# Kernel tuning notes

Hardware: AMD Instinct MI355X
Metric: run time of the kernel (lower is better)

Reference implementation:

```python
import jax, jax.numpy as jnp
import numpy as np

N = 50000   # nodes
E = 800000  # edges (before self loops)
IN_DIM = 64
HID = 128
HEADS = 4
DH = HID // HEADS  # 32 per-head out_feats
L = 3
EPS = 1e-5
NEG_SLOPE = 0.2


def setup_inputs() -> dict:
    key = jax.random.key(0)
    ks = jax.random.split(key, 10)
    s = 0.1  # weight scale for numerical sanity
    return {
        "node_feats": jax.random.normal(ks[0], (N, IN_DIM), jnp.float32),
        "src": jax.random.randint(ks[1], (E,), 0, N, dtype=jnp.int32),
        "dst": jax.random.randint(ks[2], (E,), 0, N, dtype=jnp.int32),
        "W_in": jax.random.normal(ks[3], (IN_DIM, HID), jnp.float32) * s,
        "b_in": jnp.zeros((HID,), jnp.float32),
        "W_src": jax.random.normal(ks[4], (L, HID, HID), jnp.float32) * s,
        "b_src": jnp.zeros((L, HID), jnp.float32),
        "W_dst": jax.random.normal(ks[5], (L, HID, HID), jnp.float32) * s,
        "b_dst": jnp.zeros((L, HID), jnp.float32),
        "attn": jax.random.normal(ks[6], (L, HEADS, DH), jnp.float32) * s,
        "ln_g": jnp.ones((L, HID), jnp.float32),
        "ln_b": jnp.zeros((L, HID), jnp.float32),
    }


def _layer_norm(x, g, b):
    mu = jnp.mean(x, axis=-1, keepdims=True)
    var = jnp.mean((x - mu) ** 2, axis=-1, keepdims=True)
    return (x - mu) * jax.lax.rsqrt(var + EPS) * g + b


def _gatv2(h, s_idx, d_idx, Ws, bs, Wd, bd, a):
    # h: [N, HID]; edges s_idx -> d_idx (self loops included)
    fs = (h @ Ws + bs).reshape(N, HEADS, DH)  # W_src h, source features
    fd = (h @ Wd + bd).reshape(N, HEADS, DH)  # W_dst h, dest features
    e = jax.nn.leaky_relu(fs[s_idx] + fd[d_idx], NEG_SLOPE)   # [E', H, D]
    logits = jnp.einsum('ehd,hd->eh', e, a)                   # [E', H]
    # segment softmax over incoming edges of each destination node
    m = jax.ops.segment_max(logits, d_idx, num_segments=N)    # [N, H]
    p = jnp.exp(logits - m[d_idx])
    z = jax.ops.segment_sum(p, d_idx, num_segments=N)         # [N, H]
    alpha = p / z[d_idx]                                      # [E', H]
    msg = fs[s_idx] * alpha[..., None]                        # [E', H, D]
    out = jax.ops.segment_sum(msg, d_idx, num_segments=N)     # [N, H, D]
    out = out + h.reshape(N, HEADS, DH)  # residual (Identity res_fc)
    return out.reshape(N, HID)


def reference(node_feats, src, dst, W_in, b_in, W_src, b_src, W_dst, b_dst, attn, ln_g, ln_b):
    loop = jnp.arange(N, dtype=src.dtype)
    s_idx = jnp.concatenate([src, loop])  # add_self_loop
    d_idx = jnp.concatenate([dst, loop])
    h = node_feats @ W_in + b_in
    for l in range(L):
        h_new = _gatv2(h, s_idx, d_idx, W_src[l], b_src[l], W_dst[l], b_dst[l], attn[l])
        h = _layer_norm(h + h_new, ln_g[l], ln_b[l])
        h = jax.nn.relu(h)
    graph_emb = jnp.mean(h, axis=0, keepdims=True)  # dgl.mean_nodes, batch of 1 graph
    return graph_emb, h
```

## Files before the change

kernel.cpp:

```cpp
#include <hip/hip_runtime.h>
#include <hip/hip_bf16.h>

#define NN 50000
#define CSTRIDE 16

typedef short short8 __attribute__((ext_vector_type(8)));
typedef float f32x4 __attribute__((ext_vector_type(4)));

#define GLOBAL_AS __attribute__((address_space(1)))
#define LDS_AS __attribute__((address_space(3)))

__device__ __forceinline__ unsigned short f2bf(float f) {
    unsigned int b = __float_as_uint(f);
    unsigned int r = (b + 0x7FFFu + ((b >> 16) & 1u)) >> 16;
    return (unsigned short)r;
}
__device__ __forceinline__ float bf2f(unsigned short u) {
    return __uint_as_float((unsigned int)u << 16);
}


__global__ __launch_bounds__(256, 4) void prep_kernel(
        const int* __restrict__ dst, int* countsS, int* __restrict__ rank, int E,
        const float* __restrict__ Ws, const float* __restrict__ Wd,
        unsigned short* __restrict__ WtL,
        const float* __restrict__ x, const float* __restrict__ Win,
        const float* __restrict__ bin, unsigned short* __restrict__ hB) {
    int HB = (E + 255) >> 8;
    int blk = blockIdx.x;
    if (blk < HB) {
        int i = blk * 256 + threadIdx.x;
        if (i < E) rank[i] = atomicAdd(&countsS[(size_t)dst[i] * CSTRIDE], 1);
        return;
    }
    if (blk < HB + 384) {
        int e = (blk - HB) * 256 + threadIdx.x;
        int l = e >> 15;
        int r = e & 32767;
        int colc = r >> 7;
        int k = r & 127;
        float v = (colc < 128) ? Ws[l * 16384 + k * 128 + colc]
                               : Wd[l * 16384 + k * 128 + (colc - 128)];
        WtL[l * 32768 + colc * 128 + k] = f2bf(v);
        return;
    }
    int blk0 = blk - HB - 384;
    int tid = threadIdx.x;
    int w = tid >> 6, l = tid & 63;
    int m = l & 15, q = l >> 4;
    short8 B[2][2];
    #pragma unroll
    for (int ct = 0; ct < 2; ++ct) {
        int colw = w * 32 + ct * 16 + m;
        #pragma unroll
        for (int kt = 0; kt < 2; ++kt) {
            short8 a;
            #pragma unroll
            for (int jj = 0; jj < 8; ++jj)
                a[jj] = (short)f2bf(Win[(kt * 32 + q * 8 + jj) * 128 + colw]);
            B[ct][kt] = a;
        }
    }
    float bias[2];
    #pragma unroll
    for (int ct = 0; ct < 2; ++ct) bias[ct] = bin[w * 32 + ct * 16 + m];
    for (int rg = blk0; rg < NN / 16; rg += 512) {
        int row0 = rg * 16;
        const float* ap = x + (size_t)(row0 + m) * 64 + q * 8;
        short8 A[2];
        #pragma unroll
        for (int kt = 0; kt < 2; ++kt) {
            float4 f0 = *(const float4*)(ap + kt * 32);
            float4 f1 = *(const float4*)(ap + kt * 32 + 4);
            short8 a;
            a[0] = (short)f2bf(f0.x); a[1] = (short)f2bf(f0.y);
            a[2] = (short)f2bf(f0.z); a[3] = (short)f2bf(f0.w);
            a[4] = (short)f2bf(f1.x); a[5] = (short)f2bf(f1.y);
            a[6] = (short)f2bf(f1.z); a[7] = (short)f2bf(f1.w);
            A[kt] = a;
        }
        f32x4 acc[2];
        #pragma unroll
        for (int ct = 0; ct < 2; ++ct) acc[ct] = (f32x4){0.f, 0.f, 0.f, 0.f};
        #pragma unroll
        for (int kt = 0; kt < 2; ++kt)
            #pragma unroll
            for (int ct = 0; ct < 2; ++ct)
                acc[ct] = __builtin_amdgcn_mfma_f32_16x16x32_bf16(A[kt], B[ct][kt], acc[ct], 0, 0, 0);
        #pragma unroll
        for (int ct = 0; ct < 2; ++ct) {
            int colw = w * 32 + ct * 16 + m;
            #pragma unroll
            for (int i = 0; i < 4; ++i) {
                int row = row0 + q * 4 + i;
                hB[(size_t)row * 128 + colw] = f2bf(acc[ct][i] + bias[ct]);
            }
        }
    }
}

__global__ __launch_bounds__(256) void alloc_kernel(const int* __restrict__ countsS,
                                                    int* __restrict__ row_beg,
                                                    int* total, int n) {
    int i = blockIdx.x * blockDim.x + threadIdx.x;
    int lane = threadIdx.x & 63;
    int len = (i < n) ? (countsS[(size_t)i * CSTRIDE] + 1) : 0;
    int p = len;
    #pragma unroll
    for (int off = 1; off < 64; off <<= 1) {
        int t = __shfl_up(p, off);
        if (lane >= off) p += t;
    }
    int tot = __shfl(p, 63);
    int base = 0;
    if (lane == 63) base = atomicAdd(total, tot);
    base = __shfl(base, 63);
    if (i < n) row_beg[i] = base + p - len;
}

__device__ __forceinline__ void dual_body(const unsigned short* __restrict__ hB,
                                          const unsigned short* __restrict__ Wt,
                                          const float* __restrict__ bs,
                                          const float* __restrict__ bd,
                                          unsigned short* __restrict__ fsB,
                                          unsigned short* __restrict__ fdB,
                                          unsigned short* Atile, int t0, int tstride) {
    int tid = threadIdx.x;
    int w = tid >> 6, l = tid & 63;
    int m = l & 15, q = l >> 4;
    short8 B[4][4];
    #pragma unroll
    for (int ct = 0; ct < 4; ++ct) {
        int colw = w * 64 + ct * 16 + m;
        const unsigned short* wp = Wt + colw * 128 + q * 8;
        #pragma unroll
        for (int kt = 0; kt < 4; ++kt) B[ct][kt] = *(const short8*)(wp + kt * 32);
    }
    const float* bptr = (w < 2) ? bs : bd;
    unsigned short* OUT = (w < 2) ? fsB : fdB;
    int ocb = (w * 64) & 127;
    float bias[4];
    #pragma unroll
    for (int ct = 0; ct < 4; ++ct) bias[ct] = bptr[ocb + ct * 16 + m];

    const int NT = (NN + 63) / 64;
    for (int t = t0; t < NT; t += tstride) {
        int row0 = t * 64;
        const char* gsrc = (const char*)(hB + (size_t)row0 * 128);
        #pragma unroll
        for (int c = 0; c < 4; ++c) {
            int off = c * 4096 + tid * 16;
            __builtin_amdgcn_global_load_lds((const GLOBAL_AS void*)(gsrc + off),
                                             (LDS_AS void*)((char*)Atile + off), 16, 0, 0);
        }
        __syncthreads();
        #pragma unroll
        for (int rg = 0; rg < 4; ++rg) {
            const unsigned short* ap = Atile + (rg * 16 + m) * 128 + q * 8;
            short8 A[4];
            #pragma unroll
            for (int kt = 0; kt < 4; ++kt) A[kt] = *(const short8*)(ap + kt * 32);
            f32x4 acc[4];
            #pragma unroll
            for (int ct = 0; ct < 4; ++ct) acc[ct] = (f32x4){0.f, 0.f, 0.f, 0.f};
            #pragma unroll
            for (int kt = 0; kt < 4; ++kt)
                #pragma unroll
                for (int ct = 0; ct < 4; ++ct)
                    acc[ct] = __builtin_amdgcn_mfma_f32_16x16x32_bf16(A[kt], B[ct][kt], acc[ct], 0, 0, 0);
            #pragma unroll
            for (int ct = 0; ct < 4; ++ct) {
                int colw = ocb + ct * 16 + m;
                #pragma unroll
                for (int i = 0; i < 4; ++i) {
                    int row = row0 + rg * 16 + q * 4 + i;
                    if (row < NN) OUT[(size_t)row * 128 + colw] = f2bf(acc[ct][i] + bias[ct]);
                }
            }
        }
        __syncthreads();
    }
}

__global__ __launch_bounds__(256, 4) void scatter_dual_kernel(
        const int* __restrict__ src, const int* __restrict__ dst,
        const int* __restrict__ rank, const int* __restrict__ row_beg,
        const int* __restrict__ countsS, int* __restrict__ col, int E, int n,
        const unsigned short* __restrict__ hB, const unsigned short* __restrict__ Wt,
        const float* __restrict__ bs, const float* __restrict__ bd,
        unsigned short* __restrict__ fsB, unsigned short* __restrict__ fdB) {
    __shared__ unsigned short Atile[64 * 128];
    int SB = (E + n + 255) >> 8;
    if ((int)blockIdx.x < SB) {
        int i = blockIdx.x * 256 + threadIdx.x;
        if (i >= E + n) return;
        if (i < E) {
            col[row_beg[dst[i]] + rank[i]] = src[i];
        } else {
            int v = i - E;
            col[row_beg[v] + countsS[(size_t)v * CSTRIDE]] = v;
        }
        return;
    }
    dual_body(hB, Wt, bs, bd, fsB, fdB, Atile, blockIdx.x - SB, gridDim.x - SB);
}

__global__ __launch_bounds__(256, 4) void dual_gemm_mfma(const unsigned short* __restrict__ hB,
                                                         const unsigned short* __restrict__ Wt,
                                                         const float* __restrict__ bs,
                                                         const float* __restrict__ bd,
                                                         unsigned short* __restrict__ fsB,
                                                         unsigned short* __restrict__ fdB) {
    __shared__ unsigned short Atile[64 * 128];
    dual_body(hB, Wt, bs, bd, fsB, fdB, Atile, blockIdx.x, gridDim.x);
}

__global__ __launch_bounds__(256) void agg_ln_kernel(const unsigned short* __restrict__ h_in,
                                                     const unsigned short* __restrict__ fsB,
                                                     const unsigned short* __restrict__ fdB,
                                                     const int* __restrict__ row_beg,
                                                     const int* __restrict__ countsS,
                                                     const int* __restrict__ col,
                                                     const float* __restrict__ attn,
                                                     const float* __restrict__ ln_g,
                                                     const float* __restrict__ ln_b,
                                                     unsigned short* __restrict__ hb_out,
                                                     float* __restrict__ hf_out, int n) {
    int gwave = (blockIdx.x * blockDim.x + threadIdx.x) >> 6;
    int lane = threadIdx.x & 63;
    int half = lane >> 5;
    int sub = lane & 31;
    int node = gwave * 2 + half;
    if (node >= n) return;
    int f0 = 4 * sub;
    unsigned foff = (unsigned)(f0 * 2);
    const char* fsp = (const char*)fsB;
    ushort4 ud = *(const ushort4*)((const char*)fdB + (((unsigned)node << 8) | foff));
    float4 fd4;
    fd4.x = bf2f(ud.x); fd4.y = bf2f(ud.y); fd4.z = bf2f(ud.z); fd4.w = bf2f(ud.w);
    ushort4 uh = *(const ushort4*)((const char*)h_in + (((unsigned)node << 8) | foff));
    float4 h4;
    h4.x = bf2f(uh.x); h4.y = bf2f(uh.y); h4.z = bf2f(uh.z); h4.w = bf2f(uh.w);
    const float4 a4 = *(const float4*)(attn + f0);
    float4 a06, a04;
    a06.x = 0.6f * a4.x; a06.y = 0.6f * a4.y; a06.z = 0.6f * a4.z; a06.w = 0.6f * a4.w;
    a04.x = 0.4f * a4.x; a04.y = 0.4f * a4.y; a04.z = 0.4f * a4.z; a04.w = 0.4f * a4.w;
    int beg = row_beg[node], end = beg + countsS[(size_t)node * CSTRIDE] + 1;

    float z[4];
    float4 acc[4];
    #pragma unroll
    for (int k = 0; k < 4; ++k) {
        z[k] = 0.f;
        acc[k].x = 0.f; acc[k].y = 0.f; acc[k].z = 0.f; acc[k].w = 0.f;
    }

    int j = beg;
    for (; j + 3 < end; j += 4) {
        int s0 = col[j], s1 = col[j + 1], s2 = col[j + 2], s3 = col[j + 3];
        ushort4 u0 = *(const ushort4*)(fsp + (((unsigned)s0 << 8) | foff));
        ushort4 u1 = *(const ushort4*)(fsp + (((unsigned)s1 << 8) | foff));
        ushort4 u2 = *(const ushort4*)(fsp + (((unsigned)s2 << 8) | foff));
        ushort4 u3 = *(const ushort4*)(fsp + (((unsigned)s3 << 8) | foff));
        float4 v0, v1, v2, v3;
        v0.x = bf2f(u0.x); v0.y = bf2f(u0.y); v0.z = bf2f(u0.z); v0.w = bf2f(u0.w);
        v1.x = bf2f(u1.x); v1.y = bf2f(u1.y); v1.z = bf2f(u1.z); v1.w = bf2f(u1.w);
        v2.x = bf2f(u2.x); v2.y = bf2f(u2.y); v2.z = bf2f(u2.z); v2.w = bf2f(u2.w);
        v3.x = bf2f(u3.x); v3.y = bf2f(u3.y); v3.z = bf2f(u3.z); v3.w = bf2f(u3.w);
        float p0, p1, p2, p3;
        {
            float e0 = v0.x + fd4.x, e1 = v0.y + fd4.y, e2 = v0.z + fd4.z, e3 = v0.w + fd4.w;
            p0 = e0 * a06.x + fabsf(e0) * a04.x + e1 * a06.y + fabsf(e1) * a04.y
               + e2 * a06.z + fabsf(e2) * a04.z + e3 * a06.w + fabsf(e3) * a04.w;
        }
        {
            float e0 = v1.x + fd4.x, e1 = v1.y + fd4.y, e2 = v1.z + fd4.z, e3 = v1.w + fd4.w;
            p1 = e0 * a06.x + fabsf(e0) * a04.x + e1 * a06.y + fabsf(e1) * a04.y
               + e2 * a06.z + fabsf(e2) * a04.z + e3 * a06.w + fabsf(e3) * a04.w;
        }
        {
            float e0 = v2.x + fd4.x, e1 = v2.y + fd4.y, e2 = v2.z + fd4.z, e3 = v2.w + fd4.w;
            p2 = e0 * a06.x + fabsf(e0) * a04.x + e1 * a06.y + fabsf(e1) * a04.y
               + e2 * a06.z + fabsf(e2) * a04.z + e3 * a06.w + fabsf(e3) * a04.w;
        }
        {
            float e0 = v3.x + fd4.x, e1 = v3.y + fd4.y, e2 = v3.z + fd4.z, e3 = v3.w + fd4.w;
            p3 = e0 * a06.x + fabsf(e0) * a04.x + e1 * a06.y + fabsf(e1) * a04.y
               + e2 * a06.z + fabsf(e2) * a04.z + e3 * a06.w + fabsf(e3) * a04.w;
        }
        #pragma unroll
        for (int off = 1; off <= 4; off <<= 1) {
            p0 += __shfl_xor(p0, off);
            p1 += __shfl_xor(p1, off);
            p2 += __shfl_xor(p2, off);
            p3 += __shfl_xor(p3, off);
        }
        float w0 = __expf(p0), w1 = __expf(p1), w2 = __expf(p2), w3 = __expf(p3);
        z[0] += w0; z[1] += w1; z[2] += w2; z[3] += w3;
        acc[0].x += w0 * v0.x; acc[0].y += w0 * v0.y; acc[0].z += w0 * v0.z; acc[0].w += w0 * v0.w;
        acc[1].x += w1 * v1.x; acc[1].y += w1 * v1.y; acc[1].z += w1 * v1.z; acc[1].w += w1 * v1.w;
        acc[2].x += w2 * v2.x; acc[2].y += w2 * v2.y; acc[2].z += w2 * v2.z; acc[2].w += w2 * v2.w;
        acc[3].x += w3 * v3.x; acc[3].y += w3 * v3.y; acc[3].z += w3 * v3.z; acc[3].w += w3 * v3.w;
    }
    for (; j < end; ++j) {
        int s = col[j];
        ushort4 u = *(const ushort4*)(fsp + (((unsigned)s << 8) | foff));
        float4 v;
        v.x = bf2f(u.x); v.y = bf2f(u.y); v.z = bf2f(u.z); v.w = bf2f(u.w);
        float e0 = v.x + fd4.x, e1 = v.y + fd4.y, e2 = v.z + fd4.z, e3 = v.w + fd4.w;
        float p = e0 * a06.x + fabsf(e0) * a04.x + e1 * a06.y + fabsf(e1) * a04.y
                + e2 * a06.z + fabsf(e2) * a04.z + e3 * a06.w + fabsf(e3) * a04.w;
        p += __shfl_xor(p, 1);
        p += __shfl_xor(p, 2);
        p += __shfl_xor(p, 4);
        float w = __expf(p);
        z[0] += w;
        acc[0].x += w * v.x; acc[0].y += w * v.y; acc[0].z += w * v.z; acc[0].w += w * v.w;
    }
    float zT = (z[0] + z[1]) + (z[2] + z[3]);
    float axT = (acc[0].x + acc[1].x) + (acc[2].x + acc[3].x);
    float ayT = (acc[0].y + acc[1].y) + (acc[2].y + acc[3].y);
    float azT = (acc[0].z + acc[1].z) + (acc[2].z + acc[3].z);
    float awT = (acc[0].w + acc[1].w) + (acc[2].w + acc[3].w);
    float inv = 1.0f / zT;
    float x0 = 2.f * h4.x + axT * inv;
    float x1 = 2.f * h4.y + ayT * inv;
    float x2 = 2.f * h4.z + azT * inv;
    float x3 = 2.f * h4.w + awT * inv;
    float s = (x0 + x1) + (x2 + x3);
    #pragma unroll
    for (int off = 1; off <= 16; off <<= 1) s += __shfl_xor(s, off);
    float mean = s * (1.f / 128.f);
    float d0 = x0 - mean, d1 = x1 - mean, d2 = x2 - mean, d3 = x3 - mean;
    float v = (d0 * d0 + d1 * d1) + (d2 * d2 + d3 * d3);
    #pragma unroll
    for (int off = 1; off <= 16; off <<= 1) v += __shfl_xor(v, off);
    float rstd = rsqrtf(v * (1.f / 128.f) + 1e-5f);
    float4 g4 = *(const float4*)(ln_g + f0);
    float4 bb4 = *(const float4*)(ln_b + f0);
    float4 o;
    o.x = fmaxf(d0 * rstd * g4.x + bb4.x, 0.f);
    o.y = fmaxf(d1 * rstd * g4.y + bb4.y, 0.f);
    o.z = fmaxf(d2 * rstd * g4.z + bb4.z, 0.f);
    o.w = fmaxf(d3 * rstd * g4.w + bb4.w, 0.f);
    if (hf_out) {
        *(float4*)((char*)hf_out + (((unsigned)node << 9) | (unsigned)(f0 * 4))) = o;
    } else {
        ushort4 ob;
        ob.x = f2bf(o.x); ob.y = f2bf(o.y); ob.z = f2bf(o.z); ob.w = f2bf(o.w);
        *(ushort4*)((char*)hb_out + (((unsigned)node << 8) | foff)) = ob;
    }
}


__global__ __launch_bounds__(128) void mean1_kernel(const float* __restrict__ h,
                                                    float* __restrict__ partials, int n) {
    int c = threadIdx.x;
    float acc = 0.f;
    for (int r = blockIdx.x; r < n; r += gridDim.x)
        acc += h[(size_t)r * 128 + c];
    partials[blockIdx.x * 128 + c] = acc;
}

__global__ __launch_bounds__(1024) void mean2_kernel(const float* __restrict__ partials,
                                                     float* __restrict__ out, int nb, int n) {
    __shared__ float smem[8][128];
    int c = threadIdx.x & 127;
    int g = threadIdx.x >> 7;
    float acc = 0.f;
    for (int r = g; r < nb; r += 8)
        acc += partials[r * 128 + c];
    smem[g][c] = acc;
    __syncthreads();
    if (threadIdx.x < 128) {
        float s = 0.f;
        #pragma unroll
        for (int k = 0; k < 8; ++k) s += smem[k][c];
        out[c] = s * (1.f / n);
    }
}

extern "C" void kernel_launch(void* const* d_in, const int* in_sizes, int n_in,
                              void* d_out, int out_size, void* d_ws, size_t ws_size,
                              hipStream_t stream) {
    const float* node_feats = (const float*)d_in[0];
    const int* src = (const int*)d_in[1];
    const int* dst = (const int*)d_in[2];
    const float* W_in = (const float*)d_in[3];
    const float* b_in = (const float*)d_in[4];
    const float* W_src = (const float*)d_in[5];
    const float* b_src = (const float*)d_in[6];
    const float* W_dst = (const float*)d_in[7];
    const float* b_dst = (const float*)d_in[8];
    const float* attn = (const float*)d_in[9];
    const float* ln_g = (const float*)d_in[10];
    const float* ln_b = (const float*)d_in[11];
    float* out = (float*)d_out;

    const int N = NN;
    const int E = in_sizes[1];

    unsigned short* fsB = (unsigned short*)d_ws;
    unsigned short* fdB = fsB + (size_t)N * 128;
    unsigned short* hB = fdB + (size_t)N * 128;
    unsigned short* WtL = hB + (size_t)N * 128;
    unsigned short* WtIn = WtL + 3 * 32768;
    int* countsS = (int*)(WtIn + 8192);
    int* total = countsS + (size_t)N * CSTRIDE;
    int* row_beg = total + 1;
    int* rankb = row_beg + N;
    int* colb = rankb + E;
    float* partials = (float*)(colb + (E + N));

    const int NT = (N + 63) / 64;

    hipMemsetAsync(countsS, 0, ((size_t)N * CSTRIDE + 1) * sizeof(int), stream);
    int HB = (E + 255) / 256;
    prep_kernel<<<HB + 384 + 512, 256, 0, stream>>>(dst, countsS, rankb, E,
                                                    W_src, W_dst, WtL,
                                                    node_feats, W_in, b_in, hB);
    alloc_kernel<<<(N + 255) / 256, 256, 0, stream>>>(countsS, row_beg, total, N);

    int SB = (E + N + 255) / 256;
    scatter_dual_kernel<<<SB + NT, 256, 0, stream>>>(src, dst, rankb, row_beg,
                                                     countsS, colb, E, N,
                                                     hB, WtL, b_src, b_dst, fsB, fdB);

    for (int l = 0; l < 3; ++l) {
        int last = (l == 2);
        if (l > 0)
            dual_gemm_mfma<<<NT, 256, 0, stream>>>(hB, WtL + (size_t)l * 32768,
                                                   b_src + l * 128, b_dst + l * 128,
                                                   fsB, fdB);
        agg_ln_kernel<<<(N + 7) / 8, 256, 0, stream>>>(hB, fsB, fdB, row_beg, countsS, colb,
                                                       attn + l * 128, ln_g + l * 128,
                                                       ln_b + l * 128,
                                                       last ? nullptr : hB,
                                                       last ? (out + 128) : nullptr, N);
    }

    mean1_kernel<<<256, 128, 0, stream>>>(out + 128, partials, N);
    mean2_kernel<<<1, 1024, 0, stream>>>(partials, out, 256, N);
}
```

Measured before the change: 411.1 us.

## Fuse layer-0 projection into prep kernel, unroll edge loop by 8, merge mean kernels

The layer-0 dual GEMM moves into the first prep kernel. Those blocks recompute the input projection for their 64-row tile into shared memory and multiply it by W_src/W_dst read directly from fp32, so it no longer waits on the scatter kernel. The scatter becomes a standalone kernel. The aggregation loop gets an 8-edge unrolled stage to raise memory-level parallelism on the gathers. The two-stage mean reduction is replaced by one kernel that uses atomics on a zeroed output, which drops a launch but makes the summation order nondeterministic.

Measured after the change: 436.4 us. 6.1% more time.

```diff
diff --git a/kernel.cpp b/kernel.cpp
--- a/kernel.cpp
+++ b/kernel.cpp
@@ -18,82 +18,205 @@
 __device__ __forceinline__ float bf2f(unsigned short u) {
     return __uint_as_float((unsigned int)u << 16);
 }
-
-
-__global__ __launch_bounds__(256, 4) void prep_kernel(
+__device__ __forceinline__ float4 bfu4(ushort4 u) {
+    float4 v;
+    v.x = bf2f(u.x); v.y = bf2f(u.y); v.z = bf2f(u.z); v.w = bf2f(u.w);
+    return v;
+}
+__device__ __forceinline__ float edge_logit(float4 v, float4 fd4, float4 a06, float4 a04) {
+    float e0 = v.x + fd4.x, e1 = v.y + fd4.y, e2 = v.z + fd4.z, e3 = v.w + fd4.w;
+    return e0 * a06.x + fabsf(e0) * a04.x + e1 * a06.y + fabsf(e1) * a04.y
+         + e2 * a06.z + fabsf(e2) * a04.z + e3 * a06.w + fabsf(e3) * a04.w;
+}
+
+
+__global__ __launch_bounds__(256, 4) void mega0_kernel(
         const int* __restrict__ dst, int* countsS, int* __restrict__ rank, int E,
         const float* __restrict__ Ws, const float* __restrict__ Wd,
         unsigned short* __restrict__ WtL,
         const float* __restrict__ x, const float* __restrict__ Win,
-        const float* __restrict__ bin, unsigned short* __restrict__ hB) {
+        const float* __restrict__ bin, unsigned short* __restrict__ hB,
+        const float* __restrict__ bs0, const float* __restrict__ bd0,
+        unsigned short* __restrict__ fsB, unsigned short* __restrict__ fdB) {
+    __shared__ unsigned short Atile[64 * 128];
     int HB = (E + 255) >> 8;
     int blk = blockIdx.x;
+    int tid = threadIdx.x;
     if (blk < HB) {
-        int i = blk * 256 + threadIdx.x;
+        int i = blk * 256 + tid;
         if (i < E) rank[i] = atomicAdd(&countsS[(size_t)dst[i] * CSTRIDE], 1);
         return;
     }
-    if (blk < HB + 384) {
-        int e = (blk - HB) * 256 + threadIdx.x;
-        int l = e >> 15;
+    int w = tid >> 6, l = tid & 63;
+    int m = l & 15, q = l >> 4;
+    if (blk < HB + 512) {
+        int blk0 = blk - HB;
+        short8 B[2][2];
+        #pragma unroll
+        for (int ct = 0; ct < 2; ++ct) {
+            int colw = w * 32 + ct * 16 + m;
+            #pragma unroll
+            for (int kt = 0; kt < 2; ++kt) {
+                short8 a;
+                #pragma unroll
+                for (int jj = 0; jj < 8; ++jj)
+                    a[jj] = (short)f2bf(Win[(kt * 32 + q * 8 + jj) * 128 + colw]);
+                B[ct][kt] = a;
+            }
+        }
+        float bias[2];
+        #pragma unroll
+        for (int ct = 0; ct < 2; ++ct) bias[ct] = bin[w * 32 + ct * 16 + m];
+        for (int rg = blk0; rg < NN / 16; rg += 512) {
+            int row0 = rg * 16;
+            const float* ap = x + (size_t)(row0 + m) * 64 + q * 8;
+            short8 A[2];
+            #pragma unroll
+            for (int kt = 0; kt < 2; ++kt) {
+                float4 f0 = *(const float4*)(ap + kt * 32);
+                float4 f1 = *(const float4*)(ap + kt * 32 + 4);
+                short8 a;
+                a[0] = (short)f2bf(f0.x); a[1] = (short)f2bf(f0.y);
+                a[2] = (short)f2bf(f0.z); a[3] = (short)f2bf(f0.w);
+                a[4] = (short)f2bf(f1.x); a[5] = (short)f2bf(f1.y);
+                a[6] = (short)f2bf(f1.z); a[7] = (short)f2bf(f1.w);
+                A[kt] = a;
+            }
+            f32x4 acc[2];
+            #pragma unroll
+            for (int ct = 0; ct < 2; ++ct) acc[ct] = (f32x4){0.f, 0.f, 0.f, 0.f};
+            #pragma unroll
+            for (int kt = 0; kt < 2; ++kt)
+                #pragma unroll
+                for (int ct = 0; ct < 2; ++ct)
+                    acc[ct] = __builtin_amdgcn_mfma_f32_16x16x32_bf16(A[kt], B[ct][kt], acc[ct], 0, 0, 0);
+            #pragma unroll
+            for (int ct = 0; ct < 2; ++ct) {
+                int colw = w * 32 + ct * 16 + m;
+                #pragma unroll
+                for (int i = 0; i < 4; ++i) {
+                    int row = row0 + q * 4 + i;
+                    hB[(size_t)row * 128 + colw] = f2bf(acc[ct][i] + bias[ct]);
+                }
+            }
+        }
+        return;
+    }
+    if (blk < HB + 512 + 256) {
+        int e = (blk - HB - 512) * 256 + tid;
+        int ll = 1 + (e >> 15);
         int r = e & 32767;
         int colc = r >> 7;
         int k = r & 127;
-        float v = (colc < 128) ? Ws[l * 16384 + k * 128 + colc]
-                               : Wd[l * 16384 + k * 128 + (colc - 128)];
-        WtL[l * 32768 + colc * 128 + k] = f2bf(v);
+        float v = (colc < 128) ? Ws[ll * 16384 + k * 128 + colc]
+                               : Wd[ll * 16384 + k * 128 + (colc - 128)];
+        WtL[ll * 32768 + colc * 128 + k] = f2bf(v);
         return;
     }
-    int blk0 = blk - HB - 384;
-    int tid = threadIdx.x;
-    int w = tid >> 6, l = tid & 63;
-    int m = l & 15, q = l >> 4;
-    short8 B[2][2];
-    #pragma unroll
-    for (int ct = 0; ct < 2; ++ct) {
-        int colw = w * 32 + ct * 16 + m;
-        #pragma unroll
-        for (int kt = 0; kt < 2; ++kt) {
-            short8 a;
-            #pragma unroll
-            for (int jj = 0; jj < 8; ++jj)
-                a[jj] = (short)f2bf(Win[(kt * 32 + q * 8 + jj) * 128 + colw]);
-            B[ct][kt] = a;
-        }
-    }
-    float bias[2];
-    #pragma unroll
-    for (int ct = 0; ct < 2; ++ct) bias[ct] = bin[w * 32 + ct * 16 + m];
-    for (int rg = blk0; rg < NN / 16; rg += 512) {
-        int row0 = rg * 16;
-        const float* ap = x + (size_t)(row0 + m) * 64 + q * 8;
-        short8 A[2];
-        #pragma unroll
-        for (int kt = 0; kt < 2; ++kt) {
-            float4 f0 = *(const float4*)(ap + kt * 32);
-            float4 f1 = *(const float4*)(ap + kt * 32 + 4);
-            short8 a;
-            a[0] = (short)f2bf(f0.x); a[1] = (short)f2bf(f0.y);
-            a[2] = (short)f2bf(f0.z); a[3] = (short)f2bf(f0.w);
-            a[4] = (short)f2bf(f1.x); a[5] = (short)f2bf(f1.y);
-            a[6] = (short)f2bf(f1.z); a[7] = (short)f2bf(f1.w);
-            A[kt] = a;
-        }
-        f32x4 acc[2];
-        #pragma unroll
-        for (int ct = 0; ct < 2; ++ct) acc[ct] = (f32x4){0.f, 0.f, 0.f, 0.f};
-        #pragma unroll
-        for (int kt = 0; kt < 2; ++kt)
-            #pragma unroll
-            for (int ct = 0; ct < 2; ++ct)
-                acc[ct] = __builtin_amdgcn_mfma_f32_16x16x32_bf16(A[kt], B[ct][kt], acc[ct], 0, 0, 0);
+    int t = blk - (HB + 512 + 256);
+    int row0 = t * 64;
+    {
+        short8 BW[2][2];
         #pragma unroll
         for (int ct = 0; ct < 2; ++ct) {
             int colw = w * 32 + ct * 16 + m;
             #pragma unroll
-            for (int i = 0; i < 4; ++i) {
-                int row = row0 + q * 4 + i;
-                hB[(size_t)row * 128 + colw] = f2bf(acc[ct][i] + bias[ct]);
+            for (int kt = 0; kt < 2; ++kt) {
+                short8 a;
+                #pragma unroll
+                for (int jj = 0; jj < 8; ++jj)
+                    a[jj] = (short)f2bf(Win[(kt * 32 + q * 8 + jj) * 128 + colw]);
+                BW[ct][kt] = a;
+            }
+        }
+        float biasW[2];
+        #pragma unroll
+        for (int ct = 0; ct < 2; ++ct) biasW[ct] = bin[w * 32 + ct * 16 + m];
+        #pragma unroll
+        for (int rg = 0; rg < 4; ++rg) {
+            int row = row0 + rg * 16 + m;
+            short8 A1[2];
+            if (row < NN) {
+                const float* ap = x + (size_t)row * 64 + q * 8;
+                #pragma unroll
+                for (int kt = 0; kt < 2; ++kt) {
+                    float4 f0 = *(const float4*)(ap + kt * 32);
+                    float4 f1 = *(const float4*)(ap + kt * 32 + 4);
+                    short8 a;
+                    a[0] = (short)f2bf(f0.x); a[1] = (short)f2bf(f0.y);
+                    a[2] = (short)f2bf(f0.z); a[3] = (short)f2bf(f0.w);
+                    a[4] = (short)f2bf(f1.x); a[5] = (short)f2bf(f1.y);
+                    a[6] = (short)f2bf(f1.z); a[7] = (short)f2bf(f1.w);
+                    A1[kt] = a;
+                }
+            } else {
+                #pragma unroll
+                for (int kt = 0; kt < 2; ++kt) {
+                    short8 a;
+                    #pragma unroll
+                    for (int jj = 0; jj < 8; ++jj) a[jj] = 0;
+                    A1[kt] = a;
+                }
+            }
+            f32x4 acc2[2];
+            #pragma unroll
+            for (int ct = 0; ct < 2; ++ct) acc2[ct] = (f32x4){0.f, 0.f, 0.f, 0.f};
+            #pragma unroll
+            for (int kt = 0; kt < 2; ++kt)
+                #pragma unroll
+                for (int ct = 0; ct < 2; ++ct)
+                    acc2[ct] = __builtin_amdgcn_mfma_f32_16x16x32_bf16(A1[kt], BW[ct][kt], acc2[ct], 0, 0, 0);
+            #pragma unroll
+            for (int ct = 0; ct < 2; ++ct)
+                #pragma unroll
+                for (int i = 0; i < 4; ++i)
+                    Atile[(rg * 16 + q * 4 + i) * 128 + w * 32 + ct * 16 + m] =
+                        f2bf(acc2[ct][i] + biasW[ct]);
+        }
+    }
+    __syncthreads();
+    {
+        const float* Wsel = (w < 2) ? Ws : Wd;
+        unsigned short* OUT = (w < 2) ? fsB : fdB;
+        const float* bptr = (w < 2) ? bs0 : bd0;
+        int ocb = (w * 64) & 127;
+        short8 B[4][4];
+        #pragma unroll
+        for (int ct = 0; ct < 4; ++ct) {
+            int colc = ocb + ct * 16 + m;
+            #pragma unroll
+            for (int kt = 0; kt < 4; ++kt) {
+                short8 a;
+                #pragma unroll
+                for (int jj = 0; jj < 8; ++jj)
+                    a[jj] = (short)f2bf(Wsel[(q * 8 + kt * 32 + jj) * 128 + colc]);
+                B[ct][kt] = a;
+            }
+        }
+        float bias[4];
+        #pragma unroll
+        for (int ct = 0; ct < 4; ++ct) bias[ct] = bptr[ocb + ct * 16 + m];
+        #pragma unroll
+        for (int rg = 0; rg < 4; ++rg) {
+            const unsigned short* ap = Atile + (rg * 16 + m) * 128 + q * 8;
+            short8 A[4];
+            #pragma unroll
+            for (int kt = 0; kt < 4; ++kt) A[kt] = *(const short8*)(ap + kt * 32);
+            f32x4 acc[4];
+            #pragma unroll
+            for (int ct = 0; ct < 4; ++ct) acc[ct] = (f32x4){0.f, 0.f, 0.f, 0.f};
+            #pragma unroll
+            for (int kt = 0; kt < 4; ++kt)
+                #pragma unroll
+                for (int ct = 0; ct < 4; ++ct)
+                    acc[ct] = __builtin_amdgcn_mfma_f32_16x16x32_bf16(A[kt], B[ct][kt], acc[ct], 0, 0, 0);
+            #pragma unroll
+            for (int ct = 0; ct < 4; ++ct) {
+                #pragma unroll
+                for (int i = 0; i < 4; ++i) {
+                    int row = row0 + rg * 16 + q * 4 + i;
+                    if (row < NN) OUT[(size_t)row * 128 + ocb + ct * 16 + m] = f2bf(acc[ct][i] + bias[ct]);
+                }
             }
         }
     }
@@ -118,13 +241,27 @@
     if (i < n) row_beg[i] = base + p - len;
 }
 
-__device__ __forceinline__ void dual_body(const unsigned short* __restrict__ hB,
-                                          const unsigned short* __restrict__ Wt,
-                                          const float* __restrict__ bs,
-                                          const float* __restrict__ bd,
-                                          unsigned short* __restrict__ fsB,
-                                          unsigned short* __restrict__ fdB,
-                                          unsigned short* Atile, int t0, int tstride) {
+__global__ void scatter_kernel(const int* __restrict__ src, const int* __restrict__ dst,
+                               const int* __restrict__ rank, const int* __restrict__ row_beg,
+                               const int* __restrict__ countsS,
+                               int* __restrict__ col, int E, int n) {
+    int i = blockIdx.x * blockDim.x + threadIdx.x;
+    if (i >= E + n) return;
+    if (i < E) {
+        col[row_beg[dst[i]] + rank[i]] = src[i];
+    } else {
+        int v = i - E;
+        col[row_beg[v] + countsS[(size_t)v * CSTRIDE]] = v;
+    }
+}
+
+__global__ __launch_bounds__(256, 4) void dual_gemm_mfma(const unsigned short* __restrict__ hB,
+                                                         const unsigned short* __restrict__ Wt,
+                                                         const float* __restrict__ bs,
+                                                         const float* __restrict__ bd,
+                                                         unsigned short* __restrict__ fsB,
+                                                         unsigned short* __restrict__ fdB) {
+    __shared__ unsigned short Atile[64 * 128];
     int tid = threadIdx.x;
     int w = tid >> 6, l = tid & 63;
     int m = l & 15, q = l >> 4;
@@ -144,7 +281,7 @@
     for (int ct = 0; ct < 4; ++ct) bias[ct] = bptr[ocb + ct * 16 + m];
 
     const int NT = (NN + 63) / 64;
-    for (int t = t0; t < NT; t += tstride) {
+    for (int t = blockIdx.x; t < NT; t += gridDim.x) {
         int row0 = t * 64;
         const char* gsrc = (const char*)(hB + (size_t)row0 * 128);
         #pragma unroll
@@ -180,39 +317,6 @@
         }
         __syncthreads();
     }
-}
-
-__global__ __launch_bounds__(256, 4) void scatter_dual_kernel(
-        const int* __restrict__ src, const int* __restrict__ dst,
-        const int* __restrict__ rank, const int* __restrict__ row_beg,
-        const int* __restrict__ countsS, int* __restrict__ col, int E, int n,
-        const unsigned short* __restrict__ hB, const unsigned short* __restrict__ Wt,
-        const float* __restrict__ bs, const float* __restrict__ bd,
-        unsigned short* __restrict__ fsB, unsigned short* __restrict__ fdB) {
-    __shared__ unsigned short Atile[64 * 128];
-    int SB = (E + n + 255) >> 8;
-    if ((int)blockIdx.x < SB) {
-        int i = blockIdx.x * 256 + threadIdx.x;
-        if (i >= E + n) return;
-        if (i < E) {
-            col[row_beg[dst[i]] + rank[i]] = src[i];
-        } else {
-            int v = i - E;
-            col[row_beg[v] + countsS[(size_t)v * CSTRIDE]] = v;
-        }
-        return;
-    }
-    dual_body(hB, Wt, bs, bd, fsB, fdB, Atile, blockIdx.x - SB, gridDim.x - SB);
-}
-
-__global__ __launch_bounds__(256, 4) void dual_gemm_mfma(const unsigned short* __restrict__ hB,
-                                                         const unsigned short* __restrict__ Wt,
-                                                         const float* __restrict__ bs,
-                                                         const float* __restrict__ bd,
-                                                         unsigned short* __restrict__ fsB,
-                                                         unsigned short* __restrict__ fdB) {
-    __shared__ unsigned short Atile[64 * 128];
-    dual_body(hB, Wt, bs, bd, fsB, fdB, Atile, blockIdx.x, gridDim.x);
 }
 
 __global__ __launch_bounds__(256) void agg_ln_kernel(const unsigned short* __restrict__ h_in,
@@ -235,12 +339,8 @@
     int f0 = 4 * sub;
     unsigned foff = (unsigned)(f0 * 2);
     const char* fsp = (const char*)fsB;
-    ushort4 ud = *(const ushort4*)((const char*)fdB + (((unsigned)node << 8) | foff));
-    float4 fd4;
-    fd4.x = bf2f(ud.x); fd4.y = bf2f(ud.y); fd4.z = bf2f(ud.z); fd4.w = bf2f(ud.w);
-    ushort4 uh = *(const ushort4*)((const char*)h_in + (((unsigned)node << 8) | foff));
-    float4 h4;
-    h4.x = bf2f(uh.x); h4.y = bf2f(uh.y); h4.z = bf2f(uh.z); h4.w = bf2f(uh.w);
+    float4 fd4 = bfu4(*(const ushort4*)((const char*)fdB + (((unsigned)node << 8) | foff)));
+    float4 h4 = bfu4(*(const ushort4*)((const char*)h_in + (((unsigned)node << 8) | foff)));
     const float4 a4 = *(const float4*)(attn + f0);
     float4 a06, a04;
     a06.x = 0.6f * a4.x; a06.y = 0.6f * a4.y; a06.z = 0.6f * a4.z; a06.w = 0.6f * a4.w;
@@ -256,44 +356,62 @@
     }
 
     int j = beg;
+    for (; j + 7 < end; j += 8) {
+        int s0 = col[j], s1 = col[j + 1], s2 = col[j + 2], s3 = col[j + 3];
+        int s4 = col[j + 4], s5 = col[j + 5], s6 = col[j + 6], s7 = col[j + 7];
+        ushort4 u0 = *(const ushort4*)(fsp + (((unsigned)s0 << 8) | foff));
+        ushort4 u1 = *(const ushort4*)(fsp + (((unsigned)s1 << 8) | foff));
+        ushort4 u2 = *(const ushort4*)(fsp + (((unsigned)s2 << 8) | foff));
+        ushort4 u3 = *(const ushort4*)(fsp + (((unsigned)s3 << 8) | foff));
+        ushort4 u4 = *(const ushort4*)(fsp + (((unsigned)s4 << 8) | foff));
+        ushort4 u5 = *(const ushort4*)(fsp + (((unsigned)s5 << 8) | foff));
+        ushort4 u6 = *(const ushort4*)(fsp + (((unsigned)s6 << 8) | foff));
+        ushort4 u7 = *(const ushort4*)(fsp + (((unsigned)s7 << 8) | foff));
+        float4 v0 = bfu4(u0), v1 = bfu4(u1), v2 = bfu4(u2), v3 = bfu4(u3);
+        float4 v4 = bfu4(u4), v5 = bfu4(u5), v6 = bfu4(u6), v7 = bfu4(u7);
+        float p0 = edge_logit(v0, fd4, a06, a04);
+        float p1 = edge_logit(v1, fd4, a06, a04);
+        float p2 = edge_logit(v2, fd4, a06, a04);
+        float p3 = edge_logit(v3, fd4, a06, a04);
+        float p4 = edge_logit(v4, fd4, a06, a04);
+        float p5 = edge_logit(v5, fd4, a06, a04);
+        float p6 = edge_logit(v6, fd4, a06, a04);
+        float p7 = edge_logit(v7, fd4, a06, a04);
+        #pragma unroll
+        for (int off = 1; off <= 4; off <<= 1) {
+            p0 += __shfl_xor(p0, off); p1 += __shfl_xor(p1, off);
+            p2 += __shfl_xor(p2, off); p3 += __shfl_xor(p3, off);
+            p4 += __shfl_xor(p4, off); p5 += __shfl_xor(p5, off);
+            p6 += __shfl_xor(p6, off); p7 += __shfl_xor(p7, off);
+        }
+        float w0 = __expf(p0), w1 = __expf(p1), w2 = __expf(p2), w3 = __expf(p3);
+        float w4 = __expf(p4), w5 = __expf(p5), w6 = __expf(p6), w7 = __expf(p7);
+        z[0] += w0; z[1] += w1; z[2] += w2; z[3] += w3;
+        z[0] += w4; z[1] += w5; z[2] += w6; z[3] += w7;
+        acc[0].x += w0 * v0.x; acc[0].y += w0 * v0.y; acc[0].z += w0 * v0.z; acc[0].w += w0 * v0.w;
+        acc[1].x += w1 * v1.x; acc[1].y += w1 * v1.y; acc[1].z += w1 * v1.z; acc[1].w += w1 * v1.w;
+        acc[2].x += w2 * v2.x; acc[2].y += w2 * v2.y; acc[2].z += w2 * v2.z; acc[2].w += w2 * v2.w;
+        acc[3].x += w3 * v3.x; acc[3].y += w3 * v3.y; acc[3].z += w3 * v3.z; acc[3].w += w3 * v3.w;
+        acc[0].x += w4 * v4.x; acc[0].y += w4 * v4.y; acc[0].z += w4 * v4.z; acc[0].w += w4 * v4.w;
+        acc[1].x += w5 * v5.x; acc[1].y += w5 * v5.y; acc[1].z += w5 * v5.z; acc[1].w += w5 * v5.w;
+        acc[2].x += w6 * v6.x; acc[2].y += w6 * v6.y; acc[2].z += w6 * v6.z; acc[2].w += w6 * v6.w;
+        acc[3].x += w7 * v7.x; acc[3].y += w7 * v7.y; acc[3].z += w7 * v7.z; acc[3].w += w7 * v7.w;
+    }
     for (; j + 3 < end; j += 4) {
         int s0 = col[j], s1 = col[j + 1], s2 = col[j + 2], s3 = col[j + 3];
         ushort4 u0 = *(const ushort4*)(fsp + (((unsigned)s0 << 8) | foff));
         ushort4 u1 = *(const ushort4*)(fsp + (((unsigned)s1 << 8) | foff));
         ushort4 u2 = *(const ushort4*)(fsp + (((unsigned)s2 << 8) | foff));
         ushort4 u3 = *(const ushort4*)(fsp + (((unsigned)s3 << 8) | foff));
-        float4 v0, v1, v2, v3;
-        v0.x = bf2f(u0.x); v0.y = bf2f(u0.y); v0.z = bf2f(u0.z); v0.w = bf2f(u0.w);
-        v1.x = bf2f(u1.x); v1.y = bf2f(u1.y); v1.z = bf2f(u1.z); v1.w = bf2f(u1.w);
-        v2.x = bf2f(u2.x); v2.y = bf2f(u2.y); v2.z = bf2f(u2.z); v2.w = bf2f(u2.w);
-        v3.x = bf2f(u3.x); v3.y = bf2f(u3.y); v3.z = bf2f(u3.z); v3.w = bf2f(u3.w);
-        float p0, p1, p2, p3;
-        {
-            float e0 = v0.x + fd4.x, e1 = v0.y + fd4.y, e2 = v0.z + fd4.z, e3 = v0.w + fd4.w;
-            p0 = e0 * a06.x + fabsf(e0) * a04.x + e1 * a06.y + fabsf(e1) * a04.y
-               + e2 * a06.z + fabsf(e2) * a04.z + e3 * a06.w + fabsf(e3) * a04.w;
-        }
-        {
-            float e0 = v1.x + fd4.x, e1 = v1.y + fd4.y, e2 = v1.z + fd4.z, e3 = v1.w + fd4.w;
-            p1 = e0 * a06.x + fabsf(e0) * a04.x + e1 * a06.y + fabsf(e1) * a04.y
-               + e2 * a06.z + fabsf(e2) * a04.z + e3 * a06.w + fabsf(e3) * a04.w;
-        }
-        {
-            float e0 = v2.x + fd4.x, e1 = v2.y + fd4.y, e2 = v2.z + fd4.z, e3 = v2.w + fd4.w;
-            p2 = e0 * a06.x + fabsf(e0) * a04.x + e1 * a06.y + fabsf(e1) * a04.y
-               + e2 * a06.z + fabsf(e2) * a04.z + e3 * a06.w + fabsf(e3) * a04.w;
-        }
-        {
-            float e0 = v3.x + fd4.x, e1 = v3.y + fd4.y, e2 = v3.z + fd4.z, e3 = v3.w + fd4.w;
-            p3 = e0 * a06.x + fabsf(e0) * a04.x + e1 * a06.y + fabsf(e1) * a04.y
-               + e2 * a06.z + fabsf(e2) * a04.z + e3 * a06.w + fabsf(e3) * a04.w;
-        }
+        float4 v0 = bfu4(u0), v1 = bfu4(u1), v2 = bfu4(u2), v3 = bfu4(u3);
+        float p0 = edge_logit(v0, fd4, a06, a04);
+        float p1 = edge_logit(v1, fd4, a06, a04);
+        float p2 = edge_logit(v2, fd4, a06, a04);
+        float p3 = edge_logit(v3, fd4, a06, a04);
         #pragma unroll
         for (int off = 1; off <= 4; off <<= 1) {
-            p0 += __shfl_xor(p0, off);
-            p1 += __shfl_xor(p1, off);
-            p2 += __shfl_xor(p2, off);
-            p3 += __shfl_xor(p3, off);
+            p0 += __shfl_xor(p0, off); p1 += __shfl_xor(p1, off);
+            p2 += __shfl_xor(p2, off); p3 += __shfl_xor(p3, off);
         }
         float w0 = __expf(p0), w1 = __expf(p1), w2 = __expf(p2), w3 = __expf(p3);
         z[0] += w0; z[1] += w1; z[2] += w2; z[3] += w3;
@@ -305,11 +423,8 @@
     for (; j < end; ++j) {
         int s = col[j];
         ushort4 u = *(const ushort4*)(fsp + (((unsigned)s << 8) | foff));
-        float4 v;
-        v.x = bf2f(u.x); v.y = bf2f(u.y); v.z = bf2f(u.z); v.w = bf2f(u.w);
-        float e0 = v.x + fd4.x, e1 = v.y + fd4.y, e2 = v.z + fd4.z, e3 = v.w + fd4.w;
-        float p = e0 * a06.x + fabsf(e0) * a04.x + e1 * a06.y + fabsf(e1) * a04.y
-                + e2 * a06.z + fabsf(e2) * a04.z + e3 * a06.w + fabsf(e3) * a04.w;
+        float4 v = bfu4(u);
+        float p = edge_logit(v, fd4, a06, a04);
         p += __shfl_xor(p, 1);
         p += __shfl_xor(p, 2);
         p += __shfl_xor(p, 4);
@@ -352,32 +467,13 @@
     }
 }
 
-
-__global__ __launch_bounds__(128) void mean1_kernel(const float* __restrict__ h,
-                                                    float* __restrict__ partials, int n) {
+__global__ __launch_bounds__(128) void mean_kernel(const float* __restrict__ h,
+                                                   float* __restrict__ out, int n) {
     int c = threadIdx.x;
     float acc = 0.f;
     for (int r = blockIdx.x; r < n; r += gridDim.x)
         acc += h[(size_t)r * 128 + c];
-    partials[blockIdx.x * 128 + c] = acc;
-}
-
-__global__ __launch_bounds__(1024) void mean2_kernel(const float* __restrict__ partials,
-                                                     float* __restrict__ out, int nb, int n) {
-    __shared__ float smem[8][128];
-    int c = threadIdx.x & 127;
-    int g = threadIdx.x >> 7;
-    float acc = 0.f;
-    for (int r = g; r < nb; r += 8)
-        acc += partials[r * 128 + c];
-    smem[g][c] = acc;
-    __syncthreads();
-    if (threadIdx.x < 128) {
-        float s = 0.f;
-        #pragma unroll
-        for (int k = 0; k < 8; ++k) s += smem[k][c];
-        out[c] = s * (1.f / n);
-    }
+    atomicAdd(&out[c], acc * (1.f / n));
 }
 
 extern "C" void kernel_launch(void* const* d_in, const int* in_sizes, int n_in,
@@ -410,21 +506,20 @@
     int* row_beg = total + 1;
     int* rankb = row_beg + N;
     int* colb = rankb + E;
-    float* partials = (float*)(colb + (E + N));
 
     const int NT = (N + 63) / 64;
 
     hipMemsetAsync(countsS, 0, ((size_t)N * CSTRIDE + 1) * sizeof(int), stream);
+    hipMemsetAsync(out, 0, 128 * sizeof(float), stream);
+
     int HB = (E + 255) / 256;
-    prep_kernel<<<HB + 384 + 512, 256, 0, stream>>>(dst, countsS, rankb, E,
-                                                    W_src, W_dst, WtL,
-                                                    node_feats, W_in, b_in, hB);
+    mega0_kernel<<<HB + 512 + 256 + NT, 256, 0, stream>>>(
+        dst, countsS, rankb, E, W_src, W_dst, WtL,
+        node_feats, W_in, b_in, hB, b_src, b_dst, fsB, fdB);
+
     alloc_kernel<<<(N + 255) / 256, 256, 0, stream>>>(countsS, row_beg, total, N);
-
-    int SB = (E + N + 255) / 256;
-    scatter_dual_kernel<<<SB + NT, 256, 0, stream>>>(src, dst, rankb, row_beg,
-                                                     countsS, colb, E, N,
-                                                     hB, WtL, b_src, b_dst, fsB, fdB);
+    scatter_kernel<<<(E + N + 255) / 256, 256, 0, stream>>>(src, dst, rankb, row_beg,
+                                                            countsS, colb, E, N);
 
     for (int l = 0; l < 3; ++l) {
         int last = (l == 2);
@@ -439,6 +534,5 @@
                                                        last ? (out + 128) : nullptr, N);
     }
 
-    mean1_kernel<<<256, 128, 0, stream>>>(out + 128, partials, N);
-    mean2_kernel<<<1, 1024, 0, stream>>>(partials, out, 256, N);
-}
+    mean_kernel<<<256, 128, 0, stream>>>(out + 128, out, N);
+}
```
